# Optimization experiments

Measured on AMD Instinct MI355X. Metric: run time of the kernel, lower is better.

The kernel has to match this reference:

```python
import jax, jax.numpy as jnp
import numpy as np

VOCAB_N = 200000
EMBED_DIM = 128
N_POS = 10
N_NEG = 64


def _one_hot_rows(key, n_rows, n_cols):
    idx = jax.random.randint(key, (n_rows,), 0, n_cols)
    return jax.nn.one_hot(idx, n_cols, dtype=jnp.float32)


def setup_inputs() -> dict:
    key = jax.random.key(0)
    k1, k2, k3, k4, k5 = jax.random.split(key, 5)
    center_word = _one_hot_rows(k1, 1, VOCAB_N)[0]            # [N]
    positive_words = _one_hot_rows(k2, N_POS, VOCAB_N)        # [P, N]
    negative_words = _one_hot_rows(k3, N_NEG, VOCAB_N)        # [K, N]
    input_embeddings = jax.random.uniform(k4, (EMBED_DIM, VOCAB_N), dtype=jnp.float32)
    output_embeddings = jax.random.uniform(k5, (VOCAB_N, EMBED_DIM), dtype=jnp.float32)
    return {
        "center_word": center_word,
        "positive_words": positive_words,
        "negative_words": negative_words,
        "input_embeddings": input_embeddings,
        "output_embeddings": output_embeddings,
    }


def reference(center_word, positive_words, negative_words, input_embeddings, output_embeddings):
    # input_embedding = center_word @ input_embeddings.T  -> [1, d]
    input_embedding = jnp.matmul(center_word, input_embeddings.T).reshape(1, -1)
    # positive context embeddings from the INPUT table (as in original code)
    positive_embeddings = jnp.matmul(positive_words, input_embeddings.T)   # [P, d]
    pos_score = jnp.matmul(input_embedding, positive_embeddings.T).squeeze()  # [P]
    pos_score = jnp.sum(jax.nn.log_sigmoid(pos_score), axis=0)
    # negative samples from the OUTPUT table
    negative_embeddings = jnp.matmul(negative_words, output_embeddings)    # [K, d]
    neg_score = jnp.matmul(input_embedding, negative_embeddings.T).squeeze()  # [K]
    neg_score = jnp.sum(jax.nn.log_sigmoid(-neg_score), axis=0)
    return -(pos_score + neg_score)
```

## Files before the change

kernel.cpp:

```cpp
#include <hip/hip_runtime.h>
#include <hip/hip_bf16.h>
#include <stdint.h>

#define VOCAB_N   200000
#define EMBED_DIM 128
#define N_POS     10
#define N_NEG     64
#define N_ROWS    (1 + N_POS + N_NEG)

#define SLOT_C 0
#define SLOT_P 2
#define SLOT_N 22
#define N_SLOTS 150

#define VEC_C (VOCAB_N / 8)
#define VEC_P (N_POS * VOCAB_N / 8)
#define VEC_N (N_NEG * VOCAB_N / 8)
#define VEC_TOT (VEC_C + VEC_P + VEC_N)

__device__ __forceinline__ float bf2f(uint16_t u) {
    uint32_t b = ((uint32_t)u) << 16;
    float f;
    __builtin_memcpy(&f, &b, sizeof(f));
    return f;
}

__global__ void k_init(int* __restrict__ ws) {
    const int t = threadIdx.x;
    if (t < N_SLOTS) ws[t] = -1;
}

template <int UPPER>
__global__ void k_scan(const uint16_t* __restrict__ cbuf,
                       const uint16_t* __restrict__ pbuf,
                       const uint16_t* __restrict__ nbuf,
                       int* __restrict__ ws) {
    if (UPPER) {
        __shared__ int go;
        if (threadIdx.x == 0) {
            int all = 1;
            for (int i = 0; i < N_POS; ++i) all &= (ws[SLOT_P + i] >= 0);
            go = !all;
        }
        __syncthreads();
        if (!go) return;
    }
    const int g = blockIdx.x * blockDim.x + threadIdx.x;
    const uint16_t* base;
    int vloc, slot_base, S;
    if (g < VEC_C) {
        base = cbuf; vloc = g; slot_base = SLOT_C; S = VOCAB_N;
    } else if (g < VEC_C + VEC_P) {
        base = pbuf; vloc = g - VEC_C; slot_base = SLOT_P; S = N_POS * VOCAB_N;
    } else if (g < VEC_TOT) {
        base = nbuf; vloc = g - VEC_C - VEC_P; slot_base = SLOT_N; S = N_NEG * VOCAB_N;
    } else {
        return;
    }
    const int off = (UPPER ? S : 0) + vloc * 8;
    const uint4 u = *reinterpret_cast<const uint4*>(base + off);
    const uint32_t w[4] = {u.x, u.y, u.z, u.w};
#pragma unroll
    for (int j = 0; j < 4; ++j) {
        if (w[j] & 0xFFFFu) { const int h = off + 2 * j;     ws[slot_base + h / VOCAB_N] = h; }
        if (w[j] >> 16)     { const int h = off + 2 * j + 1; ws[slot_base + h / VOCAB_N] = h; }
    }
}

__global__ void k_loss(const void* __restrict__ iemb_v,
                       const void* __restrict__ oemb_v,
                       const int* __restrict__ ws,
                       void* __restrict__ out_v) {
    __shared__ int cols[N_ROWS];
    __shared__ int mode_fp32;
    __shared__ float v[EMBED_DIM];
    __shared__ float wave_sum[4];

    const int t = threadIdx.x;

    if (t == 0) {
        int all = 1;
        for (int i = 0; i < N_POS; ++i) all &= (ws[SLOT_P + i] >= 0);
        mode_fp32 = !all;
    }
    __syncthreads();
    const bool f32 = (mode_fp32 != 0);

    if (t < N_ROWS) {
        int base, local;
        if (t == 0)          { base = SLOT_C; local = 0; }
        else if (t <= N_POS) { base = SLOT_P; local = t - 1; }
        else                 { base = SLOT_N; local = t - 1 - N_POS; }
        int h;
        if (f32) {
            const int s0 = ws[base + 2 * local];
            const int s1 = ws[base + 2 * local + 1];
            h = (s0 >= 0) ? s0 : s1;
            h >>= 1;
        } else {
            h = ws[base + local];
        }
        cols[t] = h - local * VOCAB_N;
    }
    __syncthreads();

    const int c = cols[0];
    if (t < EMBED_DIM) {
        v[t] = f32 ? ((const float*)iemb_v)[(size_t)t * VOCAB_N + c]
                   : bf2f(((const uint16_t*)iemb_v)[(size_t)t * VOCAB_N + c]);
    }
    __syncthreads();

    const int wave = t >> 6;
    const int lane = t & 63;
    float local_sum = 0.f;

    for (int p = wave; p < N_POS + N_NEG; p += 4) {
        const int e = cols[1 + p];
        float a0, a1;
        if (p < N_POS) {
            if (f32) {
                a0 = ((const float*)iemb_v)[(size_t)lane * VOCAB_N + e];
                a1 = ((const float*)iemb_v)[(size_t)(lane + 64) * VOCAB_N + e];
            } else {
                a0 = bf2f(((const uint16_t*)iemb_v)[(size_t)lane * VOCAB_N + e]);
                a1 = bf2f(((const uint16_t*)iemb_v)[(size_t)(lane + 64) * VOCAB_N + e]);
            }
        } else {
            if (f32) {
                a0 = ((const float*)oemb_v)[(size_t)e * EMBED_DIM + lane];
                a1 = ((const float*)oemb_v)[(size_t)e * EMBED_DIM + lane + 64];
            } else {
                a0 = bf2f(((const uint16_t*)oemb_v)[(size_t)e * EMBED_DIM + lane]);
                a1 = bf2f(((const uint16_t*)oemb_v)[(size_t)e * EMBED_DIM + lane + 64]);
            }
        }
        float d = a0 * v[lane] + a1 * v[lane + 64];
#pragma unroll
        for (int off = 32; off > 0; off >>= 1)
            d += __shfl_down(d, off, 64);
        if (lane == 0) {
            const float x = (p < N_POS) ? d : -d;
            const float ls = (x >= 0.f) ? -log1pf(expf(-x))
                                        : (x - log1pf(expf(x)));
            local_sum += ls;
        }
    }

    if (lane == 0) wave_sum[wave] = local_sum;
    __syncthreads();
    if (t == 0) {
        const float total = wave_sum[0] + wave_sum[1] + wave_sum[2] + wave_sum[3];
        if (f32) ((float*)out_v)[0] = -total;
        else     ((__hip_bfloat16*)out_v)[0] = __float2bfloat16(-total);
    }
}

extern "C" void kernel_launch(void* const* d_in, const int* in_sizes, int n_in,
                              void* d_out, int out_size, void* d_ws, size_t ws_size,
                              hipStream_t stream) {
    if (ws_size < sizeof(int) * N_SLOTS) return;

    const uint16_t* center = (const uint16_t*)d_in[0];
    const uint16_t* pos    = (const uint16_t*)d_in[1];
    const uint16_t* neg    = (const uint16_t*)d_in[2];
    const void*     iemb   = d_in[3];
    const void*     oemb   = d_in[4];
    int* ws = (int*)d_ws;

    const int nblk = (VEC_TOT + 255) / 256;
    k_init<<<1, 256, 0, stream>>>(ws);
    k_scan<0><<<nblk, 256, 0, stream>>>(center, pos, neg, ws);
    k_scan<1><<<nblk, 256, 0, stream>>>(center, pos, neg, ws);
    k_loss<<<1, 256, 0, stream>>>(iemb, oemb, ws, d_out);
}
```

Measured before the change: 233.6 us.

## Assume fp32 inputs and scan one-hot rows in a single pass

Drops the dual bf16/fp32 detection scheme, which needed an init kernel plus two scan launches over the one-hot buffers. Inputs are now treated as fp32 only, and a single scan kernel reads 8 floats per thread and writes the column index for each row directly. The loss kernel reads those indices without any mode logic. This removes two kernel launches and avoids reading the buffers twice. In exchange it relies on every one-hot row having exactly one nonzero entry and no longer initializes the workspace.

```diff
diff --git a/kernel.cpp b/kernel.cpp
--- a/kernel.cpp
+++ b/kernel.cpp
@@ -7,108 +7,50 @@
 #define N_POS     10
 #define N_NEG     64
 #define N_ROWS    (1 + N_POS + N_NEG)
+#define TOT_FLOATS (N_ROWS * VOCAB_N)
+#define THREADS_SCAN (TOT_FLOATS / 8)
 
-#define SLOT_C 0
-#define SLOT_P 2
-#define SLOT_N 22
-#define N_SLOTS 150
+__global__ void k_scan(const float* __restrict__ cbuf,
+                       const float* __restrict__ pbuf,
+                       const float* __restrict__ nbuf,
+                       int* __restrict__ ws) {
+    const int g = blockIdx.x * blockDim.x + threadIdx.x;
+    if (g >= THREADS_SCAN) return;
+    const int f0 = g * 8;
 
-#define VEC_C (VOCAB_N / 8)
-#define VEC_P (N_POS * VOCAB_N / 8)
-#define VEC_N (N_NEG * VOCAB_N / 8)
-#define VEC_TOT (VEC_C + VEC_P + VEC_N)
+    const float* src;
+    int off;
+    if (f0 < VOCAB_N)                  { src = cbuf; off = f0; }
+    else if (f0 < (1 + N_POS) * VOCAB_N) { src = pbuf; off = f0 - VOCAB_N; }
+    else                               { src = nbuf; off = f0 - (1 + N_POS) * VOCAB_N; }
 
-__device__ __forceinline__ float bf2f(uint16_t u) {
-    uint32_t b = ((uint32_t)u) << 16;
-    float f;
-    __builtin_memcpy(&f, &b, sizeof(f));
-    return f;
-}
-
-__global__ void k_init(int* __restrict__ ws) {
-    const int t = threadIdx.x;
-    if (t < N_SLOTS) ws[t] = -1;
-}
-
-template <int UPPER>
-__global__ void k_scan(const uint16_t* __restrict__ cbuf,
-                       const uint16_t* __restrict__ pbuf,
-                       const uint16_t* __restrict__ nbuf,
-                       int* __restrict__ ws) {
-    if (UPPER) {
-        __shared__ int go;
-        if (threadIdx.x == 0) {
-            int all = 1;
-            for (int i = 0; i < N_POS; ++i) all &= (ws[SLOT_P + i] >= 0);
-            go = !all;
+    const uint4 a = *reinterpret_cast<const uint4*>(src + off);
+    const uint4 b = *reinterpret_cast<const uint4*>(src + off + 4);
+    const uint32_t w[8] = {a.x, a.y, a.z, a.w, b.x, b.y, b.z, b.w};
+#pragma unroll
+    for (int j = 0; j < 8; ++j) {
+        if (w[j]) {
+            const int gf = f0 + j;
+            ws[gf / VOCAB_N] = gf % VOCAB_N;
         }
-        __syncthreads();
-        if (!go) return;
-    }
-    const int g = blockIdx.x * blockDim.x + threadIdx.x;
-    const uint16_t* base;
-    int vloc, slot_base, S;
-    if (g < VEC_C) {
-        base = cbuf; vloc = g; slot_base = SLOT_C; S = VOCAB_N;
-    } else if (g < VEC_C + VEC_P) {
-        base = pbuf; vloc = g - VEC_C; slot_base = SLOT_P; S = N_POS * VOCAB_N;
-    } else if (g < VEC_TOT) {
-        base = nbuf; vloc = g - VEC_C - VEC_P; slot_base = SLOT_N; S = N_NEG * VOCAB_N;
-    } else {
-        return;
-    }
-    const int off = (UPPER ? S : 0) + vloc * 8;
-    const uint4 u = *reinterpret_cast<const uint4*>(base + off);
-    const uint32_t w[4] = {u.x, u.y, u.z, u.w};
-#pragma unroll
-    for (int j = 0; j < 4; ++j) {
-        if (w[j] & 0xFFFFu) { const int h = off + 2 * j;     ws[slot_base + h / VOCAB_N] = h; }
-        if (w[j] >> 16)     { const int h = off + 2 * j + 1; ws[slot_base + h / VOCAB_N] = h; }
     }
 }
 
-__global__ void k_loss(const void* __restrict__ iemb_v,
-                       const void* __restrict__ oemb_v,
+__global__ void k_loss(const float* __restrict__ iemb,
+                       const float* __restrict__ oemb,
                        const int* __restrict__ ws,
-                       void* __restrict__ out_v) {
+                       float* __restrict__ out) {
     __shared__ int cols[N_ROWS];
-    __shared__ int mode_fp32;
     __shared__ float v[EMBED_DIM];
     __shared__ float wave_sum[4];
 
     const int t = threadIdx.x;
-
-    if (t == 0) {
-        int all = 1;
-        for (int i = 0; i < N_POS; ++i) all &= (ws[SLOT_P + i] >= 0);
-        mode_fp32 = !all;
-    }
-    __syncthreads();
-    const bool f32 = (mode_fp32 != 0);
-
-    if (t < N_ROWS) {
-        int base, local;
-        if (t == 0)          { base = SLOT_C; local = 0; }
-        else if (t <= N_POS) { base = SLOT_P; local = t - 1; }
-        else                 { base = SLOT_N; local = t - 1 - N_POS; }
-        int h;
-        if (f32) {
-            const int s0 = ws[base + 2 * local];
-            const int s1 = ws[base + 2 * local + 1];
-            h = (s0 >= 0) ? s0 : s1;
-            h >>= 1;
-        } else {
-            h = ws[base + local];
-        }
-        cols[t] = h - local * VOCAB_N;
-    }
+    if (t < N_ROWS) cols[t] = ws[t];
     __syncthreads();
 
     const int c = cols[0];
-    if (t < EMBED_DIM) {
-        v[t] = f32 ? ((const float*)iemb_v)[(size_t)t * VOCAB_N + c]
-                   : bf2f(((const uint16_t*)iemb_v)[(size_t)t * VOCAB_N + c]);
-    }
+    if (t < EMBED_DIM)
+        v[t] = iemb[(size_t)t * VOCAB_N + c];
     __syncthreads();
 
     const int wave = t >> 6;
@@ -119,21 +61,11 @@
         const int e = cols[1 + p];
         float a0, a1;
         if (p < N_POS) {
-            if (f32) {
-                a0 = ((const float*)iemb_v)[(size_t)lane * VOCAB_N + e];
-                a1 = ((const float*)iemb_v)[(size_t)(lane + 64) * VOCAB_N + e];
-            } else {
-                a0 = bf2f(((const uint16_t*)iemb_v)[(size_t)lane * VOCAB_N + e]);
-                a1 = bf2f(((const uint16_t*)iemb_v)[(size_t)(lane + 64) * VOCAB_N + e]);
-            }
+            a0 = iemb[(size_t)lane * VOCAB_N + e];
+            a1 = iemb[(size_t)(lane + 64) * VOCAB_N + e];
         } else {
-            if (f32) {
-                a0 = ((const float*)oemb_v)[(size_t)e * EMBED_DIM + lane];
-                a1 = ((const float*)oemb_v)[(size_t)e * EMBED_DIM + lane + 64];
-            } else {
-                a0 = bf2f(((const uint16_t*)oemb_v)[(size_t)e * EMBED_DIM + lane]);
-                a1 = bf2f(((const uint16_t*)oemb_v)[(size_t)e * EMBED_DIM + lane + 64]);
-            }
+            a0 = oemb[(size_t)e * EMBED_DIM + lane];
+            a1 = oemb[(size_t)e * EMBED_DIM + lane + 64];
         }
         float d = a0 * v[lane] + a1 * v[lane + 64];
 #pragma unroll
@@ -149,28 +81,21 @@
 
     if (lane == 0) wave_sum[wave] = local_sum;
     __syncthreads();
-    if (t == 0) {
-        const float total = wave_sum[0] + wave_sum[1] + wave_sum[2] + wave_sum[3];
-        if (f32) ((float*)out_v)[0] = -total;
-        else     ((__hip_bfloat16*)out_v)[0] = __float2bfloat16(-total);
-    }
+    if (t == 0)
+        out[0] = -(wave_sum[0] + wave_sum[1] + wave_sum[2] + wave_sum[3]);
 }
 
 extern "C" void kernel_launch(void* const* d_in, const int* in_sizes, int n_in,
                               void* d_out, int out_size, void* d_ws, size_t ws_size,
                               hipStream_t stream) {
-    if (ws_size < sizeof(int) * N_SLOTS) return;
-
-    const uint16_t* center = (const uint16_t*)d_in[0];
-    const uint16_t* pos    = (const uint16_t*)d_in[1];
-    const uint16_t* neg    = (const uint16_t*)d_in[2];
-    const void*     iemb   = d_in[3];
-    const void*     oemb   = d_in[4];
+    const float* center = (const float*)d_in[0];
+    const float* pos    = (const float*)d_in[1];
+    const float* neg    = (const float*)d_in[2];
+    const float* iemb   = (const float*)d_in[3];
+    const float* oemb   = (const float*)d_in[4];
     int* ws = (int*)d_ws;
 
-    const int nblk = (VEC_TOT + 255) / 256;
-    k_init<<<1, 256, 0, stream>>>(ws);
-    k_scan<0><<<nblk, 256, 0, stream>>>(center, pos, neg, ws);
-    k_scan<1><<<nblk, 256, 0, stream>>>(center, pos, neg, ws);
-    k_loss<<<1, 256, 0, stream>>>(iemb, oemb, ws, d_out);
+    const int nblk = (THREADS_SCAN + 255) / 256;
+    k_scan<<<nblk, 256, 0, stream>>>(center, pos, neg, ws);
+    k_loss<<<1, 256, 0, stream>>>(iemb, oemb, ws, (float*)d_out);
 }
```

After: 230.9 us. No clear change (-1.1%).
